# Optimization experiments

Hardware: AMD Instinct MI355X
Metric: run time of the kernel (lower is better)

## Reference

```python
import jax, jax.numpy as jnp
import numpy as np

E = 1024          # embed_dim
BS = 8            # number of sequences (bs = pre_lf_indexs.shape[0])
L = 8192          # tokens per sequence
N = BS * L        # packed tokens
CACHE = 16384     # lf cache rows
EPS = 1e-6


def setup_inputs() -> dict:
    key = jax.random.key(0)
    ks = jax.random.split(key, 9)
    inputs = jax.random.normal(ks[0], (N, E), jnp.float32)
    conv1_weight = jax.random.normal(ks[1], (E, E), jnp.float32) * (1.0 / np.sqrt(E))
    conv2_weight = jax.random.normal(ks[2], (E // 2, 2 * E), jnp.float32) * (1.0 / np.sqrt(E // 2))
    conv1_bias = jax.random.normal(ks[3], (E // 2,), jnp.float32) * 0.02
    conv2_bias = jax.random.normal(ks[4], (E,), jnp.float32) * 0.02
    ln_weight = jnp.ones((E,), jnp.float32)
    lf1_caches = jax.random.normal(ks[5], (CACHE, E), jnp.float32)
    lf2_caches = jax.random.normal(ks[6], (CACHE, E // 2), jnp.float32)
    # packed layout: each sequence prefixed by one cache slot -> T = N + BS rows
    offs = jnp.arange(BS, dtype=jnp.int32) * (L + 1)
    input_lf_loc = offs                                             # cache slot per seq
    inputs_loc = (offs[:, None] + 1 + jnp.arange(L, dtype=jnp.int32)[None, :]).reshape(-1)
    outputs_loc = inputs_loc - 1                                     # 2-tap causal pairing
    out_lf_loc = offs + L                                            # last token of each seq
    pre_lf_indexs = jax.random.randint(ks[7], (BS,), 0, CACHE, jnp.int32)
    out_lf_indexs = jax.random.randint(ks[8], (BS,), 0, CACHE, jnp.int32)
    return {
        'inputs': inputs, 'conv1_weight': conv1_weight, 'conv2_weight': conv2_weight,
        'conv1_bias': conv1_bias, 'conv2_bias': conv2_bias, 'ln_weight': ln_weight,
        'lf1_caches': lf1_caches, 'lf2_caches': lf2_caches,
        'pre_lf_indexs': pre_lf_indexs, 'out_lf_indexs': out_lf_indexs,
        'input_lf_loc': input_lf_loc, 'out_lf_loc': out_lf_loc,
        'inputs_loc': inputs_loc, 'outputs_loc': outputs_loc,
    }


def _fused_cat_conv2d(x, cache, W, pre_idx, in_lf_loc, in_loc, out_loc):
    # scatter cache rows + token rows into the padded buffer [N+bs, D]
    T = x.shape[0] + pre_idx.shape[0]
    xt = jnp.zeros((T, x.shape[1]), x.dtype)
    xt = xt.at[in_lf_loc].set(cache[pre_idx])   # gather from lf cache
    xt = xt.at[in_loc].set(x)
    co = xt @ W                                  # [T, 2*Dout]
    h = co.shape[1] // 2
    # shifted 2-tap causal conv: pair row j (prev) with row j+1 (cur)
    ot = co[:-1, :h] + co[1:, h:]                # [T-1, Dout]
    return ot[out_loc]                           # gather back to token order


def reference(inputs, conv1_weight, conv2_weight, conv1_bias, conv2_bias, ln_weight,
              lf1_caches, lf2_caches, pre_lf_indexs, out_lf_indexs,
              input_lf_loc, out_lf_loc, inputs_loc, outputs_loc):
    # (the index_put_ cache writes in the original are side effects for future
    #  steps only; they do not affect this call's output, so they are omitted)
    output1 = _fused_cat_conv2d(inputs, lf1_caches, conv1_weight,
                                pre_lf_indexs, input_lf_loc, inputs_loc, outputs_loc)
    output1 = output1 + conv1_bias               # [N, E/2]
    output2 = _fused_cat_conv2d(output1, lf2_caches, conv2_weight,
                                pre_lf_indexs, input_lf_loc, inputs_loc, outputs_loc)
    output2 = output2 + conv2_bias               # [N, E]
    x = output2 + inputs                         # residual
    var = jnp.mean(x * x, axis=-1, keepdims=True)
    return x * jax.lax.rsqrt(var + EPS) * ln_weight
```

## Files before the change

### kernel.cpp

```cpp
#include <hip/hip_runtime.h>
#include <hip/hip_bf16.h>


#define EDIM 1024
#define HDIM 512
#define LSEQ 8192
#define BSEQ 8
#define SEQR 8193
#define MTOT (BSEQ * SEQR)
#define XROWS 66048
#define CVTBLK (XROWS / 4)

using v8s = __attribute__((ext_vector_type(8))) short;
using v4f = __attribute__((ext_vector_type(4))) float;

__device__ __forceinline__ unsigned short f2b(float f) {
  union { float f; unsigned u; } v; v.f = f;
  unsigned r = v.u + 0x7fffu + ((v.u >> 16) & 1u);
  return (unsigned short)(r >> 16);
}
__device__ __forceinline__ float b2f(unsigned short h) {
  union { unsigned u; float f; } v; v.u = ((unsigned)h) << 16; return v.f;
}
__device__ __forceinline__ void gl_lds16(const void* g, void* l) {
  __builtin_amdgcn_global_load_lds((const __attribute__((address_space(1))) void*)g,
                                   (__attribute__((address_space(3))) void*)l, 16, 0, 0);
}

__device__ __forceinline__ void trns64(const float* __restrict__ src, int src_ld, int src_c0,
                                       unsigned short* __restrict__ dst, int dst_ld, int dst_k0,
                                       int n0, int k0, float (*t)[65], int tx, int ty) {
#pragma unroll
  for (int yy = 0; yy < 64; yy += 4)
    t[yy + ty][tx] = src[(size_t)(k0 + yy + ty) * src_ld + src_c0 + n0 + tx];
  __syncthreads();
#pragma unroll
  for (int yy = 0; yy < 64; yy += 4)
    dst[(size_t)(n0 + yy + ty) * dst_ld + dst_k0 + k0 + tx] = f2b(t[tx][yy + ty]);
}

__global__ __launch_bounds__(256) void cvt_prep(const float* __restrict__ inputs,
                                                const float* __restrict__ lf1,
                                                const float* __restrict__ lf2,
                                                const int* __restrict__ preidx,
                                                const float* __restrict__ W1,
                                                const float* __restrict__ W2,
                                                unsigned short* __restrict__ Xbf,
                                                unsigned short* __restrict__ W1c,
                                                unsigned short* __restrict__ W2c,
                                                unsigned short* __restrict__ c2b) {
  __shared__ float t[64][65];
  const int bk = blockIdx.x;
  const int tid = threadIdx.x;
  if (bk < CVTBLK) {
    const int r = bk * 4 + (tid >> 6);
    const int lane = tid & 63;
    unsigned short* dst = Xbf + (size_t)r * EDIM;
    if (r >= MTOT) {
#pragma unroll
      for (int c = lane * 4; c < EDIM; c += 256)
        *(ushort4*)&dst[c] = (ushort4){0, 0, 0, 0};
      return;
    }
    const int b = r / SEQR, rr = r % SEQR;
    const float* src = (rr == 0) ? (lf1 + (size_t)preidx[b] * EDIM)
                                 : (inputs + (size_t)(b * LSEQ + rr - 1) * EDIM);
#pragma unroll
    for (int c = lane * 4; c < EDIM; c += 256) {
      const float4 v = *(const float4*)(src + c);
      *(ushort4*)&dst[c] = (ushort4){f2b(v.x), f2b(v.y), f2b(v.z), f2b(v.w)};
    }
    return;
  }
  if (bk == CVTBLK + 512) {
    for (int c = tid; c < HDIM; c += 256)
#pragma unroll
      for (int b = 0; b < BSEQ; ++b)
        c2b[b * HDIM + c] = f2b(lf2[(size_t)preidx[b] * HDIM + c]);
    return;
  }
  const int s = bk - CVTBLK;
  const int tx = tid & 63, ty = tid >> 6;
  const int which = s >> 7, ss = s & 127;
  if (which == 0)       trns64(W1, 1024, 0,    W1c, 2048, 0,    (ss & 7) * 64,  (ss >> 3) * 64, t, tx, ty);
  else if (which == 1)  trns64(W1, 1024, 512,  W1c, 2048, 1024, (ss & 7) * 64,  (ss >> 3) * 64, t, tx, ty);
  else if (which == 2)  trns64(W2, 2048, 0,    W2c, 1024, 0,    (ss & 15) * 64, (ss >> 4) * 64, t, tx, ty);
  else                  trns64(W2, 2048, 1024, W2c, 1024, 512,  (ss & 15) * 64, (ss >> 4) * 64, t, tx, ty);
}

#define PHASE(p, boA_, off_, ra_)                                                      \
  {                                                                                    \
    v8s af[2][2];                                                                      \
    _Pragma("unroll") for (int m2 = 0; m2 < 2; ++m2)                                   \
    _Pragma("unroll") for (int kx = 0; kx < 2; ++kx)                                   \
      af[m2][kx] = *(const v8s*)&lds[(boA_) +                                          \
          ((2 * (p) + m2) * 32 + wm * 16 + lr + (off_)) * 64 +                         \
          (((kx * 2 + lk) ^ (ra_)) << 3)];                                             \
    __builtin_amdgcn_s_setprio(1);                                                     \
    _Pragma("unroll") for (int m2 = 0; m2 < 2; ++m2)                                   \
    _Pragma("unroll") for (int nc = 0; nc < 4; ++nc)                                   \
    _Pragma("unroll") for (int kx = 0; kx < 2; ++kx)                                   \
      acc[2 * (p) + m2][nc] = __builtin_amdgcn_mfma_f32_16x16x32_bf16(                 \
          af[m2][kx], bf[nc][kx], acc[2 * (p) + m2][nc], 0, 0, 0);                     \
    __builtin_amdgcn_s_setprio(0);                                                     \
  }

#undef PHASE
#define PHASE(p, boA_, off_, ra_)                                                      \
  {                                                                                    \
    v8s af[2][2];                                                                      \
    _Pragma("unroll") for (int m2 = 0; m2 < 2; ++m2)                                   \
    _Pragma("unroll") for (int kx = 0; kx < 2; ++kx)                                   \
      af[m2][kx] = *(const v8s*)&lds[(boA_) +                                          \
          ((2 * (p) + m2) * 32 + wm * 16 + lr + (off_)) * 64 +                         \
          (((kx * 4 + lk) ^ (ra_)) << 3)];                                             \
    __builtin_amdgcn_s_setprio(1);                                                     \
    _Pragma("unroll") for (int m2 = 0; m2 < 2; ++m2)                                   \
    _Pragma("unroll") for (int nc = 0; nc < 4; ++nc)                                   \
    _Pragma("unroll") for (int kx = 0; kx < 2; ++kx)                                   \
      acc[2 * (p) + m2][nc] = __builtin_amdgcn_mfma_f32_16x16x32_bf16(                 \
          af[m2][kx], bf[nc][kx], acc[2 * (p) + m2][nc], 0, 0, 0);                     \
    __builtin_amdgcn_s_setprio(0);                                                     \
  }

#define LOAD_BFR(boB_)                                                                 \
  _Pragma("unroll") for (int nc = 0; nc < 4; ++nc)                                     \
  _Pragma("unroll") for (int kx = 0; kx < 2; ++kx)                                     \
    bf[nc][kx] = *(const v8s*)&lds[(boB_) + (nc * 64 + wn * 16 + lr) * 64 +            \
                                   (((kx * 4 + lk) ^ ra7a) << 3)];

#define STEP4(boA_, off_, ra_)                                                         \
  PHASE(0, boA_, off_, ra_) PHASE(1, boA_, off_, ra_)                                  \
  PHASE(2, boA_, off_, ra_) PHASE(3, boA_, off_, ra_)

template <int K, int NT, bool SHIFTC, bool AMAP, bool TAIL, bool CSUB>
__global__ __launch_bounds__(512, 2) void gemm_pair(const unsigned short* __restrict__ A,
                                                    const unsigned short* __restrict__ B,
                                                    unsigned short* __restrict__ C,
                                                    const float* __restrict__ bias,
                                                    const unsigned short* __restrict__ c2b,
                                                    int q, int r) {
  constexpr int NH = K / 128;
  constexpr int LDA = K / 2;
  constexpr int N = NT * 256;
  constexpr int A0 = 0, A1 = 16512, B_A = 33024, B_B = 49408;
  __shared__ __align__(16) unsigned short lds[65792];

  const int h = blockIdx.x;
  const int mainB = 8 * q + r;

  if constexpr (TAIL) {
    if (h >= mainB) {
      const int tid = threadIdx.x;
      const int rr = 65536 + (h - mainB);
      const unsigned short* a = A + (size_t)rr * LDA;
      const unsigned short* wrow = B + (size_t)tid * K;
      float s = 0.f;
      for (int k = 0; k < K; k += 8) {
        const v8s av = *(const v8s*)&a[k];
        const v8s wv = *(const v8s*)&wrow[k];
#pragma unroll
        for (int j = 0; j < 8; ++j)
          s += b2f((unsigned short)av[j]) * b2f((unsigned short)wv[j]);
      }
      C[(size_t)(rr + 1) * N + tid] = f2b(s + bias[tid]);
      return;
    }
  }

  const int xcd = h & 7, idx = h >> 3;
  const int tsw = (xcd < r ? xcd * (q + 1) : r * (q + 1) + (xcd - r) * q) + idx;
  const int mt = tsw / NT, nt = tsw % NT;
  const size_t m0 = (size_t)mt * 256, n0 = (size_t)nt * 256;
  const int tid = threadIdx.x;
  const int w = tid >> 6, lane = tid & 63;
  const int wm = w >> 2, wn = w & 3;
  const int lr = lane & 15, lk = lane >> 4;
  const int ra7a = lr & 7, ra7b = (lr + 1) & 7;
  const int srow = tid >> 3, slot = tid & 7;
  const int gslot = slot ^ (srow & 7);
  const int dAB = srow * 64 + slot * 8;
  const int aBase = (int)m0 + (AMAP ? ((int)m0 >> 13) : 0);

  auto aSrc = [&](int row, int i, int sl) -> const unsigned short* {
    if (CSUB && ((row >> 13) == (row & 8191)))
      return c2b + (size_t)(row >> 13) * HDIM + i * 64 + sl * 8;
    return A + (size_t)row * LDA + i * 64 + sl * 8;
  };
  auto stageApair = [&](int dstE, int i) {
#pragma unroll
    for (int j = 0; j < 4; ++j) {
      const int rr = j * 64 + (tid >> 3);
      gl_lds16(aSrc(aBase + rr, i, (tid & 7) ^ (rr & 7)),
               &lds[dstE + rr * 64 + (tid & 7) * 8]);
    }
    if (tid < 8)
      gl_lds16(aSrc(aBase + 256, i, tid),
               &lds[dstE + 256 * 64 + tid * 8]);
  };
  auto stageB = [&](int dstE, int hh, int t) {
    const unsigned short* s = B + (size_t)(n0 + hh * 128 + srow) * K + t * 64 + gslot * 8;
    unsigned short* d = &lds[dstE + hh * 8192 + dAB];
    gl_lds16(s, d);
    gl_lds16(s + (size_t)64 * K, d + 4096);
  };

  v4f acc[8][4];
#pragma unroll
  for (int i = 0; i < 8; ++i)
#pragma unroll
    for (int j = 0; j < 4; ++j) acc[i][j] = (v4f){0.f, 0.f, 0.f, 0.f};

  stageApair(A0, 0);
  stageB(B_A, 0, 0); stageB(B_A, 1, 0);
  asm volatile("s_waitcnt vmcnt(0)" ::: "memory");
  __builtin_amdgcn_s_barrier();

#pragma unroll 1
  for (int i = 0; i < NH - 1; ++i) {
    const int boA = (i & 1) ? A1 : A0;
    const int soA = (i & 1) ? A0 : A1;
    v8s bf[4][2];
    stageB(B_B, 0, i + NH); stageB(B_B, 1, i + NH);
    stageApair(soA, i + 1);
    LOAD_BFR(B_A)
    STEP4(boA, 0, ra7a)
    asm volatile("s_waitcnt vmcnt(4)" ::: "memory");
    __builtin_amdgcn_s_barrier();
    stageB(B_A, 0, i + 1); stageB(B_A, 1, i + 1);
    LOAD_BFR(B_B)
    STEP4(boA, 1, ra7b)
    asm volatile("s_waitcnt vmcnt(0)" ::: "memory");
    __builtin_amdgcn_s_barrier();
  }
  {
    const int boA = ((NH - 1) & 1) ? A1 : A0;
    v8s bf[4][2];
    stageB(B_B, 0, 2 * NH - 1); stageB(B_B, 1, 2 * NH - 1);
    LOAD_BFR(B_A)
    STEP4(boA, 0, ra7a)
    asm volatile("s_waitcnt vmcnt(0)" ::: "memory");
    __builtin_amdgcn_s_barrier();
    LOAD_BFR(B_B)
    STEP4(boA, 1, ra7b)
  }

#pragma unroll
  for (int mr = 0; mr < 8; ++mr)
#pragma unroll
    for (int nc = 0; nc < 4; ++nc) {
      const size_t col = n0 + nc * 64 + wn * 16 + lr;
      float bv = 0.f;
      if constexpr (SHIFTC) bv = bias[col];
#pragma unroll
      for (int g = 0; g < 4; ++g) {
        const size_t row = m0 + mr * 32 + wm * 16 + lk * 4 + g + (SHIFTC ? 1 : 0);
        C[row * N + col] = f2b(acc[mr][nc][g] + bv);
      }
    }
}

__global__ __launch_bounds__(256) void epilogue_full(
    const unsigned short* __restrict__ Zo, const unsigned short* __restrict__ Xbf,
    const float* __restrict__ b2, const float* __restrict__ lnw,
    float* __restrict__ out) {
  const int u = blockIdx.x;
  const size_t rx = (size_t)u + (u >> 13) + 1;
  const int tid = threadIdx.x;
  const int j0 = tid * 4;

  const ushort4 z = *(const ushort4*)&Zo[(size_t)u * EDIM + j0];
  const ushort4 xb = *(const ushort4*)&Xbf[rx * EDIM + j0];
  const float4 bb = *(const float4*)&b2[j0];
  const float4 lw = *(const float4*)&lnw[j0];

  const float x0 = b2f(z.x) + bb.x + b2f(xb.x);
  const float x1 = b2f(z.y) + bb.y + b2f(xb.y);
  const float x2 = b2f(z.z) + bb.z + b2f(xb.z);
  const float x3 = b2f(z.w) + bb.w + b2f(xb.w);

  float ss = x0 * x0 + x1 * x1 + x2 * x2 + x3 * x3;
#pragma unroll
  for (int o = 32; o > 0; o >>= 1) ss += __shfl_xor(ss, o, 64);
  __shared__ float sp[4];
  if ((tid & 63) == 0) sp[tid >> 6] = ss;
  __syncthreads();
  const float tot = sp[0] + sp[1] + sp[2] + sp[3];
  const float scale = rsqrtf(tot * (1.0f / EDIM) + 1e-6f);

  float4 o4;
  o4.x = x0 * scale * lw.x; o4.y = x1 * scale * lw.y;
  o4.z = x2 * scale * lw.z; o4.w = x3 * scale * lw.w;
  *(float4*)&out[(size_t)u * EDIM + j0] = o4;
}

extern "C" void kernel_launch(void* const* d_in, const int* in_sizes, int n_in,
                              void* d_out, int out_size, void* d_ws, size_t ws_size,
                              hipStream_t stream) {
  const float* inputs = (const float*)d_in[0];
  const float* W1 = (const float*)d_in[1];
  const float* W2 = (const float*)d_in[2];
  const float* b1 = (const float*)d_in[3];
  const float* b2 = (const float*)d_in[4];
  const float* lnw = (const float*)d_in[5];
  const float* lf1 = (const float*)d_in[6];
  const float* lf2 = (const float*)d_in[7];
  const int* preidx = (const int*)d_in[8];
  float* out = (float*)d_out;

  char* ws = (char*)d_ws;
  unsigned short* Xbf = (unsigned short*)(ws);
  unsigned short* A2  = (unsigned short*)(ws + 135266304ULL);
  unsigned short* Zo  = (unsigned short*)(ws + 202899456ULL);
  unsigned short* W1c = (unsigned short*)(ws + 337117184ULL);
  unsigned short* W2c = (unsigned short*)(ws + 339214336ULL);
  unsigned short* c2b = (unsigned short*)(ws + 341311488ULL);

  cvt_prep<<<CVTBLK + 513, 256, 0, stream>>>(inputs, lf1, lf2, preidx, W1, W2,
                                             Xbf, W1c, W2c, c2b);
  gemm_pair<2048, 2, true, false, true, false>
      <<<519, 512, 0, stream>>>(Xbf, W1c, A2, b1, nullptr, 64, 0);
  gemm_pair<1024, 4, false, true, false, true>
      <<<1024, 512, 0, stream>>>(A2, W2c, Zo, nullptr, c2b, 128, 0);
  epilogue_full<<<BSEQ * LSEQ, 256, 0, stream>>>(Zo, Xbf, b2, lnw, out);
}
```

Before: 459.7 us.

## Add triple-buffered A pipeline GEMM kernel for first conv stage

Adds a new gemm3b kernel for the first GEMM (K=2048). It triple-buffers A tiles and double-buffers B tiles in a larger LDS allocation, and interleaves the global-to-LDS stage loads between MFMA phases so fewer waits fall on the critical path. The old pair-row A staging is replaced by plain row staging with a wider LDA over the concatenated K. gemm_pair is reduced to the second-GEMM specialization, with the TAIL and bias template paths removed. The larger LDS footprint (160KB per block) may reduce occupancy on top of the 2-block launch bound.

After: 465.4 us. Within noise of the previous version (+1.2%).

```diff
diff --git a/kernel.cpp b/kernel.cpp
--- a/kernel.cpp
+++ b/kernel.cpp
@@ -88,14 +88,13 @@
   else                  trns64(W2, 2048, 1024, W2c, 1024, 512,  (ss & 15) * 64, (ss >> 4) * 64, t, tx, ty);
 }
 
-#define PHASE(p, boA_, off_, ra_)                                                      \
+#define PH_A(p, boA_)                                                                  \
   {                                                                                    \
     v8s af[2][2];                                                                      \
     _Pragma("unroll") for (int m2 = 0; m2 < 2; ++m2)                                   \
     _Pragma("unroll") for (int kx = 0; kx < 2; ++kx)                                   \
-      af[m2][kx] = *(const v8s*)&lds[(boA_) +                                          \
-          ((2 * (p) + m2) * 32 + wm * 16 + lr + (off_)) * 64 +                         \
-          (((kx * 2 + lk) ^ (ra_)) << 3)];                                             \
+      af[m2][kx] = *(const v8s*)&lds[(boA_) + ((2 * (p) + m2) * 32 + wm * 16 + lr) * 64 + \
+                                     (((kx * 4 + lk) ^ ra7) << 3)];                    \
     __builtin_amdgcn_s_setprio(1);                                                     \
     _Pragma("unroll") for (int m2 = 0; m2 < 2; ++m2)                                   \
     _Pragma("unroll") for (int nc = 0; nc < 4; ++nc)                                   \
@@ -105,8 +104,141 @@
     __builtin_amdgcn_s_setprio(0);                                                     \
   }
 
-#undef PHASE
-#define PHASE(p, boA_, off_, ra_)                                                      \
+#define LB_A(boB_)                                                                     \
+  _Pragma("unroll") for (int nc = 0; nc < 4; ++nc)                                     \
+  _Pragma("unroll") for (int kx = 0; kx < 2; ++kx)                                     \
+    bf[nc][kx] = *(const v8s*)&lds[(boB_) + (nc * 64 + wn * 16 + lr) * 64 +            \
+                                   (((kx * 4 + lk) ^ ra7) << 3)];
+
+template <int K, int LDA, int NT, bool SHIFTC, bool TAIL>
+__global__ __launch_bounds__(512, 2) void gemm3b(const unsigned short* __restrict__ A,
+                                                 const unsigned short* __restrict__ B,
+                                                 unsigned short* __restrict__ C,
+                                                 const float* __restrict__ bias,
+                                                 int q, int r) {
+  constexpr int NTILES = K / 64;
+  constexpr int N = NT * 256;
+  __shared__ __align__(16) unsigned short lds[81920];
+
+  const int h = blockIdx.x;
+  const int mainB = 8 * q + r;
+
+  if constexpr (TAIL) {
+    if (h >= mainB) {
+      const int tid = threadIdx.x;
+      const int rr = 65536 + (h - mainB);
+      const unsigned short* a = A + (size_t)rr * LDA;
+      const unsigned short* wrow = B + (size_t)tid * K;
+      float s = 0.f;
+      for (int k = 0; k < K; k += 8) {
+        const v8s av = *(const v8s*)&a[k];
+        const v8s wv = *(const v8s*)&wrow[k];
+#pragma unroll
+        for (int j = 0; j < 8; ++j)
+          s += b2f((unsigned short)av[j]) * b2f((unsigned short)wv[j]);
+      }
+      C[(size_t)(rr + 1) * N + tid] = f2b(s + bias[tid]);
+      return;
+    }
+  }
+
+  const int xcd = h & 7, idx = h >> 3;
+  const int tsw = (xcd < r ? xcd * (q + 1) : r * (q + 1) + (xcd - r) * q) + idx;
+  const int mt = tsw / NT, nt = tsw % NT;
+  const size_t m0 = (size_t)mt * 256, n0 = (size_t)nt * 256;
+  const int tid = threadIdx.x;
+  const int w = tid >> 6, lane = tid & 63;
+  const int wm = w >> 2, wn = w & 3;
+  const int lr = lane & 15, lk = lane >> 4;
+  const int ra7 = lr & 7;
+  const int srow = tid >> 3, slot = tid & 7;
+  const int gslot = slot ^ (srow & 7);
+  const int dA = srow * 64 + slot * 8;
+  const unsigned short* bSrc = B + (size_t)(n0 + srow) * K + gslot * 8;
+
+  auto stageA = [&](int dst, int hh, int tt) {
+#pragma unroll
+    for (int hf = 0; hf < 2; ++hf) {
+      const int u = (int)m0 + hh * 128 + hf * 64 + srow;
+      gl_lds16(A + (size_t)u * LDA + tt * 64 + gslot * 8,
+               &lds[dst + hh * 8192 + hf * 4096 + dA]);
+    }
+  };
+  auto stageB = [&](int dst, int hh, int tt) {
+    const unsigned short* s = bSrc + (size_t)hh * 128 * K + (size_t)tt * 64;
+    unsigned short* d = &lds[dst + hh * 8192 + dA];
+    gl_lds16(s, d);
+    gl_lds16(s + (size_t)64 * K, d + 4096);
+  };
+
+  v4f acc[8][4];
+#pragma unroll
+  for (int i = 0; i < 8; ++i)
+#pragma unroll
+    for (int j = 0; j < 4; ++j) acc[i][j] = (v4f){0.f, 0.f, 0.f, 0.f};
+
+  stageB(49152, 0, 0); stageB(49152, 1, 0);
+  stageA(0, 0, 0);     stageA(0, 1, 0);
+  stageA(16384, 0, 1); stageA(16384, 1, 1);
+  asm volatile("s_waitcnt vmcnt(2)" ::: "memory");
+  __builtin_amdgcn_s_barrier();
+
+  int boA = 0, soA = 32768;
+  int boB = 49152, sB = 65536;
+#pragma unroll 1
+  for (int t0 = 0; t0 < NTILES - 2; ++t0) {
+    v8s bf[4][2];
+    stageB(sB, 0, t0 + 1);
+    LB_A(boB)
+    PH_A(0, boA)
+    stageB(sB, 1, t0 + 1);
+    PH_A(1, boA)
+    stageA(soA, 0, t0 + 2);
+    PH_A(2, boA)
+    stageA(soA, 1, t0 + 2);
+    PH_A(3, boA)
+    asm volatile("s_waitcnt vmcnt(4)" ::: "memory");
+    __builtin_amdgcn_s_barrier();
+    const int nboA = (boA == 32768) ? 0 : boA + 16384;
+    soA = boA; boA = nboA;
+    const int tmp = boB; boB = sB; sB = tmp;
+  }
+  {
+    v8s bf[4][2];
+    stageB(sB, 0, NTILES - 1);
+    LB_A(boB)
+    PH_A(0, boA)
+    stageB(sB, 1, NTILES - 1);
+    PH_A(1, boA)
+    PH_A(2, boA)
+    PH_A(3, boA)
+    asm volatile("s_waitcnt vmcnt(0)" ::: "memory");
+    __builtin_amdgcn_s_barrier();
+    boA = (boA == 32768) ? 0 : boA + 16384;
+    const int tmp = boB; boB = sB; sB = tmp;
+  }
+  {
+    v8s bf[4][2];
+    LB_A(boB)
+    PH_A(0, boA) PH_A(1, boA) PH_A(2, boA) PH_A(3, boA)
+  }
+
+#pragma unroll
+  for (int mr = 0; mr < 8; ++mr)
+#pragma unroll
+    for (int nc = 0; nc < 4; ++nc) {
+      const size_t col = n0 + nc * 64 + wn * 16 + lr;
+      float bv = 0.f;
+      if constexpr (SHIFTC) bv = bias[col];
+#pragma unroll
+      for (int g = 0; g < 4; ++g) {
+        const size_t row = m0 + mr * 32 + wm * 16 + lk * 4 + g + (SHIFTC ? 1 : 0);
+        C[row * N + col] = f2b(acc[mr][nc][g] + bv);
+      }
+    }
+}
+
+#define PH_P(p, boA_, off_, ra_)                                                       \
   {                                                                                    \
     v8s af[2][2];                                                                      \
     _Pragma("unroll") for (int m2 = 0; m2 < 2; ++m2)                                   \
@@ -123,21 +255,20 @@
     __builtin_amdgcn_s_setprio(0);                                                     \
   }
 
-#define LOAD_BFR(boB_)                                                                 \
+#define LB_P(boB_)                                                                     \
   _Pragma("unroll") for (int nc = 0; nc < 4; ++nc)                                     \
   _Pragma("unroll") for (int kx = 0; kx < 2; ++kx)                                     \
     bf[nc][kx] = *(const v8s*)&lds[(boB_) + (nc * 64 + wn * 16 + lr) * 64 +            \
                                    (((kx * 4 + lk) ^ ra7a) << 3)];
 
-#define STEP4(boA_, off_, ra_)                                                         \
-  PHASE(0, boA_, off_, ra_) PHASE(1, boA_, off_, ra_)                                  \
-  PHASE(2, boA_, off_, ra_) PHASE(3, boA_, off_, ra_)
-
-template <int K, int NT, bool SHIFTC, bool AMAP, bool TAIL, bool CSUB>
+#define ST_P(boA_, off_, ra_)                                                          \
+  PH_P(0, boA_, off_, ra_) PH_P(1, boA_, off_, ra_)                                    \
+  PH_P(2, boA_, off_, ra_) PH_P(3, boA_, off_, ra_)
+
+template <int K, int NT>
 __global__ __launch_bounds__(512, 2) void gemm_pair(const unsigned short* __restrict__ A,
                                                     const unsigned short* __restrict__ B,
                                                     unsigned short* __restrict__ C,
-                                                    const float* __restrict__ bias,
                                                     const unsigned short* __restrict__ c2b,
                                                     int q, int r) {
   constexpr int NH = K / 128;
@@ -147,27 +278,6 @@
   __shared__ __align__(16) unsigned short lds[65792];
 
   const int h = blockIdx.x;
-  const int mainB = 8 * q + r;
-
-  if constexpr (TAIL) {
-    if (h >= mainB) {
-      const int tid = threadIdx.x;
-      const int rr = 65536 + (h - mainB);
-      const unsigned short* a = A + (size_t)rr * LDA;
-      const unsigned short* wrow = B + (size_t)tid * K;
-      float s = 0.f;
-      for (int k = 0; k < K; k += 8) {
-        const v8s av = *(const v8s*)&a[k];
-        const v8s wv = *(const v8s*)&wrow[k];
-#pragma unroll
-        for (int j = 0; j < 8; ++j)
-          s += b2f((unsigned short)av[j]) * b2f((unsigned short)wv[j]);
-      }
-      C[(size_t)(rr + 1) * N + tid] = f2b(s + bias[tid]);
-      return;
-    }
-  }
-
   const int xcd = h & 7, idx = h >> 3;
   const int tsw = (xcd < r ? xcd * (q + 1) : r * (q + 1) + (xcd - r) * q) + idx;
   const int mt = tsw / NT, nt = tsw % NT;
@@ -180,10 +290,10 @@
   const int srow = tid >> 3, slot = tid & 7;
   const int gslot = slot ^ (srow & 7);
   const int dAB = srow * 64 + slot * 8;
-  const int aBase = (int)m0 + (AMAP ? ((int)m0 >> 13) : 0);
+  const int aBase = (int)m0 + ((int)m0 >> 13);
 
   auto aSrc = [&](int row, int i, int sl) -> const unsigned short* {
-    if (CSUB && ((row >> 13) == (row & 8191)))
+    if ((row >> 13) == (row & 8191))
       return c2b + (size_t)(row >> 13) * HDIM + i * 64 + sl * 8;
     return A + (size_t)row * LDA + i * 64 + sl * 8;
   };
@@ -223,13 +333,13 @@
     v8s bf[4][2];
     stageB(B_B, 0, i + NH); stageB(B_B, 1, i + NH);
     stageApair(soA, i + 1);
-    LOAD_BFR(B_A)
-    STEP4(boA, 0, ra7a)
+    LB_P(B_A)
+    ST_P(boA, 0, ra7a)
     asm volatile("s_waitcnt vmcnt(4)" ::: "memory");
     __builtin_amdgcn_s_barrier();
     stageB(B_A, 0, i + 1); stageB(B_A, 1, i + 1);
-    LOAD_BFR(B_B)
-    STEP4(boA, 1, ra7b)
+    LB_P(B_B)
+    ST_P(boA, 1, ra7b)
     asm volatile("s_waitcnt vmcnt(0)" ::: "memory");
     __builtin_amdgcn_s_barrier();
   }
@@ -237,12 +347,12 @@
     const int boA = ((NH - 1) & 1) ? A1 : A0;
     v8s bf[4][2];
     stageB(B_B, 0, 2 * NH - 1); stageB(B_B, 1, 2 * NH - 1);
-    LOAD_BFR(B_A)
-    STEP4(boA, 0, ra7a)
+    LB_P(B_A)
+    ST_P(boA, 0, ra7a)
     asm volatile("s_waitcnt vmcnt(0)" ::: "memory");
     __builtin_amdgcn_s_barrier();
-    LOAD_BFR(B_B)
-    STEP4(boA, 1, ra7b)
+    LB_P(B_B)
+    ST_P(boA, 1, ra7b)
   }
 
 #pragma unroll
@@ -250,12 +360,10 @@
 #pragma unroll
     for (int nc = 0; nc < 4; ++nc) {
       const size_t col = n0 + nc * 64 + wn * 16 + lr;
-      float bv = 0.f;
-      if constexpr (SHIFTC) bv = bias[col];
 #pragma unroll
       for (int g = 0; g < 4; ++g) {
-        const size_t row = m0 + mr * 32 + wm * 16 + lk * 4 + g + (SHIFTC ? 1 : 0);
-        C[row * N + col] = f2b(acc[mr][nc][g] + bv);
+        const size_t row = m0 + mr * 32 + wm * 16 + lk * 4 + g;
+        C[row * N + col] = f2b(acc[mr][nc][g]);
       }
     }
 }
@@ -318,9 +426,9 @@
 
   cvt_prep<<<CVTBLK + 513, 256, 0, stream>>>(inputs, lf1, lf2, preidx, W1, W2,
                                              Xbf, W1c, W2c, c2b);
-  gemm_pair<2048, 2, true, false, true, false>
-      <<<519, 512, 0, stream>>>(Xbf, W1c, A2, b1, nullptr, 64, 0);
-  gemm_pair<1024, 4, false, true, false, true>
-      <<<1024, 512, 0, stream>>>(A2, W2c, Zo, nullptr, c2b, 128, 0);
+  gemm3b<2048, 1024, 2, true, true>
+      <<<519, 512, 0, stream>>>(Xbf, W1c, A2, b1, 64, 0);
+  gemm_pair<1024, 4>
+      <<<1024, 512, 0, stream>>>(A2, W2c, Zo, c2b, 128, 0);
   epilogue_full<<<BSEQ * LSEQ, 256, 0, stream>>>(Zo, Xbf, b2, lnw, out);
 }
```
